# Kernel tuning notes

Hardware: AMD Instinct MI355X
Metric: run time of the kernel (lower is better)

Reference implementation:

```python
import jax, jax.numpy as jnp
import numpy as np

LAT = 4; K = 4; NP = 3 * K - 1; HID = 16; NT = 10; BOUND = 5.0
_in_deg = np.arange(1, LAT + 1)
_hd = (np.arange(HID) % (LAT - 1)) + 1
M1 = jnp.asarray((_hd[:, None] >= _in_deg[None, :]).astype(np.float32))  # [HID, LAT]
M2 = jnp.asarray((_hd[:, None] >= _hd[None, :]).astype(np.float32))      # [HID, HID]
M3 = jnp.asarray((np.repeat(_in_deg, NP)[:, None] > _hd[None, :]).astype(np.float32))  # [LAT*NP, HID]


def _subm(x, m, w, b):
    # submanifold conv: inactive inputs are zero, output restricted to active sites
    y = jax.lax.conv_general_dilated(x, w, (1, 1), 'SAME', dimension_numbers=('NHWC', 'HWIO', 'NHWC')) + b
    return jnp.where(m[..., None], y, 0.0)


def _maxpool(x, m, kh, kw):
    neg = jnp.asarray(-1e30, x.dtype)
    xm = jnp.where(m[..., None], x, neg)
    y = jax.lax.reduce_window(xm, neg, jax.lax.max, (1, kh, kw, 1), (1, kh, kw, 1), 'VALID')
    mo = jax.lax.reduce_window(m.astype(x.dtype), 0.0, jax.lax.max, (1, kh, kw), (1, kh, kw), 'VALID') > 0
    return jnp.where(mo[..., None], y, 0.0), mo


def _invconv(x, w, b, mo):
    # sparse inverse conv with kernel == stride of paired pool: non-overlapping transposed conv
    kh, kw, ci, co = w.shape
    B, h, wd, _ = x.shape
    y = jnp.einsum('bhwc,ijcd->bhiwjd', x, w).reshape(B, h * kh, wd * kw, co) + b
    return jnp.where(mo[..., None], y, 0.0)


def _rqs(x, uw, uh, ud):
    # monotonic rational-quadratic spline, identity outside [-BOUND, BOUND]
    shp = x.shape
    widths = jax.nn.softmax(uw, -1) * (2 * BOUND)
    heights = jax.nn.softmax(uh, -1) * (2 * BOUND)
    edge = jnp.full(shp + (1,), -BOUND, x.dtype)
    xk = jnp.concatenate([edge, jnp.cumsum(widths, -1) - BOUND], -1)
    yk = jnp.concatenate([edge, jnp.cumsum(heights, -1) - BOUND], -1)
    one = jnp.ones(shp + (1,), x.dtype)
    dk = jnp.concatenate([one, jax.nn.softplus(ud), one], -1)
    inside = (x >= -BOUND) & (x <= BOUND)
    xc = jnp.clip(x, -BOUND, BOUND)
    idx = jnp.clip(jnp.sum((xc[..., None] >= xk[..., :-1]).astype(jnp.int32), -1) - 1, 0, K - 1)[..., None]
    g = lambda a, i: jnp.take_along_axis(a, i, -1)[..., 0]
    x0, x1 = g(xk, idx), g(xk, idx + 1)
    y0, y1 = g(yk, idx), g(yk, idx + 1)
    d0, d1 = g(dk, idx), g(dk, idx + 1)
    dx = x1 - x0
    dy = y1 - y0
    s = dy / dx
    t = (xc - x0) / dx
    den = s + (d1 + d0 - 2 * s) * t * (1 - t)
    y = y0 + dy * (s * t * t + d0 * t * (1 - t)) / den
    ld = jnp.log(s * s * (d1 * t * t + 2 * s * t * (1 - t) + d0 * (1 - t) ** 2)) - 2 * jnp.log(den)
    return jnp.where(inside, y, x), jnp.where(inside, ld, 0.0)


def _nsf(z, fW1, fb1, fW2, fb2, fW3, fb3):
    ld_tot = jnp.zeros(z.shape[:-1], z.dtype)
    for t in range(NT):
        h = jax.nn.relu(z @ (fW1[t] * M1).T + fb1[t])
        h = jax.nn.relu(h @ (fW2[t] * M2).T + fb2[t])
        p = (h @ (fW3[t] * M3).T + fb3[t]).reshape(z.shape[:-1] + (LAT, NP))
        z, ld = _rqs(z, p[..., :K], p[..., K:2 * K], p[..., 2 * K:])
        ld_tot = ld_tot + ld.sum(-1)
        if t < NT - 1:
            z = z[..., ::-1]
    return z, ld_tot


def _forward(x, eps, w1, b1, w2, b2, w3, b3, wmu, bmu, wlv, blv, wlin, blin, u1, bu1, w4, b4, u2, bu2, w5, b5, u3, bu3, w6, b6, fW1, fb1, fW2, fb2, fW3, fb3):
    xn = jnp.transpose(x, (0, 2, 3, 1))  # NCHW -> NHWC
    m0 = jnp.any(xn != 0, axis=-1)       # active sites (spconv from_dense)
    lrelu = lambda v: jax.nn.leaky_relu(v, 0.01)
    y = lrelu(_subm(xn, m0, w1, b1))
    y, m1 = _maxpool(y, m0, 2, 2)
    y = lrelu(_subm(y, m1, w2, b2))
    y, m2 = _maxpool(y, m1, 5, 2)
    y = lrelu(_subm(y, m2, w3, b3))
    y, m3 = _maxpool(y, m2, 5, 2)        # [B, 4, 16, 32]
    mu = jnp.where(m3[..., None], y @ wmu.T + bmu, 0.0)
    logvar = jnp.where(m3[..., None], y @ wlv.T + blv, 0.0)
    std = jnp.exp(0.5 * logvar)
    z0 = mu + eps * std
    z, log_det = _nsf(z0, fW1, fb1, fW2, fb2, fW3, fb3)
    LOG2PI = 1.8378770664093453
    log_q0 = jnp.sum(-0.5 * ((z0 - mu) / std) ** 2 - jnp.log(std) - 0.5 * LOG2PI, -1)
    log_p = jnp.sum(-0.5 * z * z - 0.5 * LOG2PI, -1)
    kld_pc = log_q0 - log_det - log_p
    kld = jnp.sum(jnp.where(m3, kld_pc, 0.0), axis=(1, 2))  # index_add over batch indices
    zf = jnp.where(m3[..., None], z, 0.0)
    dec = jnp.where(m3[..., None], zf @ wlin.T + blin, 0.0)
    y = _invconv(dec, u1, bu1, m2)
    y = _subm(y, m2, w4, b4)
    y = _invconv(y, u2, bu2, m1)
    y = _subm(y, m1, w5, b5)
    y = _invconv(y, u3, bu3, m0)
    y = _subm(y, m0, w6, b6)
    out = jnp.transpose(y, (0, 3, 1, 2))  # back to NCHW like .dense()
    return out, mu, logvar, kld, zf


def setup_inputs():
    key = jax.random.key(0)
    ks = iter(jax.random.split(key, 80))
    B, C, H, W = 128, 6, 200, 128
    d = {}
    x = jax.random.normal(next(ks), (B, C, H, W), jnp.float32)
    keep = jax.random.uniform(next(ks), (B, 1, H, W)) < 0.15
    d['x'] = jnp.where(keep, x, 0.0)
    d['eps'] = jax.random.normal(next(ks), (B, 4, 16, LAT), jnp.float32)
    def p(name, shape, s=0.1):
        d[name] = jax.random.normal(next(ks), shape, jnp.float32) * s
    p('w1', (3, 3, 6, 8)); p('b1', (8,))
    p('w2', (3, 3, 8, 16)); p('b2', (16,))
    p('w3', (3, 3, 16, 32)); p('b3', (32,))
    p('wmu', (LAT, 32)); p('bmu', (LAT,))
    p('wlv', (LAT, 32)); p('blv', (LAT,))
    p('wlin', (32, LAT)); p('blin', (32,))
    p('u1', (5, 2, 32, 32)); p('bu1', (32,))
    p('w4', (3, 3, 32, 16)); p('b4', (16,))
    p('u2', (5, 2, 16, 16)); p('bu2', (16,))
    p('w5', (3, 3, 16, 8)); p('b5', (8,))
    p('u3', (2, 2, 8, 8)); p('bu3', (8,))
    p('w6', (3, 3, 8, 6)); p('b6', (6,))
    p('fW1', (NT, HID, LAT)); p('fb1', (NT, HID))
    p('fW2', (NT, HID, HID)); p('fb2', (NT, HID))
    p('fW3', (NT, LAT * NP, HID)); p('fb3', (NT, LAT * NP))
    return d


def reference(x, eps, w1, b1, w2, b2, w3, b3, wmu, bmu, wlv, blv, wlin, blin, u1, bu1, w4, b4, u2, bu2, w5, b5, u3, bu3, w6, b6, fW1, fb1, fW2, fb2, fW3, fb3):
    return _forward(x, eps, w1, b1, w2, b2, w3, b3, wmu, bmu, wlv, blv, wlin, blin, u1, bu1, w4, b4, u2, bu2, w5, b5, u3, bu3, w6, b6, fW1, fb1, fW2, fb2, fW3, fb3)
```

## Files before the change

kernel.cpp:

```cpp
#include <hip/hip_runtime.h>
#include <math.h>

constexpr int NB=128;
constexpr int NH0=200, NW0=128, NC0=6;
constexpr int NH1=100, NW1=64,  NC1=8;
constexpr int NH2=20,  NW2=32,  NC2=16;
constexpr int NH3=4,   NW3=16,  NC3=32;
constexpr int LAT=4, NPp=11, HID=16, NT=10;
constexpr float BOUNDf=5.0f;
constexpr float LOG2PI=1.8378770664093453f;

__device__ __forceinline__ float fexpf(float v){ return __expf(v); }
__device__ __forceinline__ float flogf(float v){ return __logf(v); }
__device__ __forceinline__ float softplusf(float v){ return v>20.f ? v : __logf(1.f+__expf(v)); }
__device__ __forceinline__ float lrelu(float v){ return v>0.f ? v : 0.01f*v; }

__global__ __launch_bounds__(256) void k_conv1pool(
    const float* __restrict__ x, const float* __restrict__ w1, const float* __restrict__ b1,
    float* __restrict__ y1p, unsigned char* __restrict__ m0, unsigned char* __restrict__ m1){
  __shared__ float xs[6][34][34];
  __shared__ float ws1[54][8];
  __shared__ unsigned char ms[34][34];
  int blk = blockIdx.x;
  int b  = blk / 28;
  int t  = blk % 28;
  int th = t / 4, tw = t % 4;
  int hp0 = th*16, wp0 = tw*16;
  int h0 = hp0*2 - 1, w0 = wp0*2 - 1;
  int tid = threadIdx.x;
  for (int i=tid;i<432;i+=256) ws1[i>>3][i&7] = w1[i];
  for (int i=tid;i<6*34*34;i+=256){
    int ci=i/1156; int rem=i-ci*1156; int r=rem/34, c=rem-r*34;
    int h=h0+r, w=w0+c;
    float v=0.f;
    if (h>=0 && h<NH0 && w>=0 && w<NW0) v = x[((size_t)(b*NC0+ci)*NH0+h)*NW0+w];
    xs[ci][r][c]=v;
  }
  __syncthreads();
  for (int i=tid;i<1156;i+=256){
    int r=i/34, c=i-r*34;
    bool any=false;
    #pragma unroll
    for (int ci=0;ci<6;ci++) any |= (xs[ci][r][c]!=0.f);
    ms[r][c] = any?1:0;
  }
  __syncthreads();
  for (int i=tid;i<1024;i+=256){
    int r=(i>>5)+1, c=(i&31)+1;
    int h=h0+r, w=w0+c;
    if (h<NH0) m0[(b*NH0+h)*NW0+w] = ms[r][c];
  }
  int lhp = tid>>4, lwp = tid&15;
  int hp = hp0+lhp, wp = wp0+lwp;
  if (hp < NH1){
    float best[8];
    #pragma unroll
    for (int co=0;co<8;co++) best[co]=-1e30f;
    bool many=false;
    #pragma unroll 1
    for (int i=0;i<2;i++)
    #pragma unroll 1
    for (int j=0;j<2;j++){
      int r = lhp*2+i+1, c = lwp*2+j+1;
      if (!ms[r][c]) continue;
      many=true;
      float a[8];
      #pragma unroll
      for (int co=0;co<8;co++) a[co]=b1[co];
      #pragma unroll 1
      for (int kh=0;kh<3;kh++)
      #pragma unroll 1
      for (int kw=0;kw<3;kw++){
        #pragma unroll
        for (int ci=0;ci<6;ci++){
          float v = xs[ci][r-1+kh][c-1+kw];
          const float* wv = ws1[(kh*3+kw)*6+ci];
          #pragma unroll
          for (int co=0;co<8;co++) a[co]=fmaf(v,wv[co],a[co]);
        }
      }
      #pragma unroll
      for (int co=0;co<8;co++) best[co]=fmaxf(best[co], lrelu(a[co]));
    }
    float* yp = y1p + (((size_t)b*NH1+hp)*NW1+wp)*8;
    #pragma unroll
    for (int co=0;co<8;co++) yp[co] = many?best[co]:0.f;
    m1[(b*NH1+hp)*NW1+wp] = many?1:0;
  }
}

__global__ __launch_bounds__(256) void k_conv2pool(
    const float* __restrict__ yin, const unsigned char* __restrict__ m1,
    const float* __restrict__ w2, const float* __restrict__ b2,
    float* __restrict__ yout, unsigned char* __restrict__ m2){
  __shared__ float ys[8][27][35];
  __shared__ unsigned char msl[27][35];
  __shared__ float w2s[72][16];
  __shared__ float b2s[16];
  int blk = blockIdx.x;
  int b  = blk >> 3;
  int t  = blk & 7;
  int th = t >> 1, tw = t & 1;
  int r0 = th*25 - 1, c0 = tw*32 - 1;
  int tid = threadIdx.x;
  for (int i=tid;i<1152;i+=256) w2s[i>>4][i&15] = w2[i];
  if (tid<16) b2s[tid]=b2[tid];
  for (int p=tid;p<27*34;p+=256){
    int r=p/34, c=p-(p/34)*34;
    int h1=r0+r, w1c=c0+c;
    bool ok = (h1>=0 && h1<NH1 && w1c>=0 && w1c<NW1);
    msl[r][c] = ok ? m1[(b*NH1+h1)*NW1+w1c] : 0;
    float4 v0=make_float4(0,0,0,0), v1=v0;
    if (ok){
      const float4* pp = (const float4*)(yin + (((size_t)b*NH1+h1)*NW1+w1c)*8);
      v0=pp[0]; v1=pp[1];
    }
    ys[0][r][c]=v0.x; ys[1][r][c]=v0.y; ys[2][r][c]=v0.z; ys[3][r][c]=v0.w;
    ys[4][r][c]=v1.x; ys[5][r][c]=v1.y; ys[6][r][c]=v1.z; ys[7][r][c]=v1.w;
  }
  __syncthreads();
  if (tid < 160){
    int oid = tid >> 1, coq = tid & 1;
    int co0 = coq*8;
    int lh = oid >> 4, lw = oid & 15;
    int h2 = th*5+lh, w2c = tw*16+lw;
    float best[8];
    #pragma unroll
    for (int co=0;co<8;co++) best[co]=-1e30f;
    bool many=false;
    #pragma unroll 1
    for (int i=0;i<5;i++)
    #pragma unroll 1
    for (int j=0;j<2;j++){
      int r = lh*5+i+1, c = lw*2+j+1;
      if (!msl[r][c]) continue;
      many=true;
      float a[8];
      #pragma unroll
      for (int co=0;co<8;co++) a[co]=b2s[co0+co];
      #pragma unroll 1
      for (int kh=0;kh<3;kh++)
      #pragma unroll 1
      for (int kw=0;kw<3;kw++){
        #pragma unroll
        for (int ci=0;ci<8;ci++){
          float v = ys[ci][r-1+kh][c-1+kw];
          const float* wr = w2s[(kh*3+kw)*8+ci];
          #pragma unroll
          for (int co=0;co<8;co++) a[co]=fmaf(v,wr[co0+co],a[co]);
        }
      }
      #pragma unroll
      for (int co=0;co<8;co++) best[co]=fmaxf(best[co], lrelu(a[co]));
    }
    float4 o0,o1;
    if (many){
      o0=make_float4(best[0],best[1],best[2],best[3]);
      o1=make_float4(best[4],best[5],best[6],best[7]);
    } else { o0=make_float4(0,0,0,0); o1=o0; }
    float4* op = (float4*)(yout + (((size_t)b*NH2+h2)*NW2+w2c)*16 + co0);
    op[0]=o0; op[1]=o1;
    if (coq==0) m2[(b*NH2+h2)*NW2+w2c] = many?1:0;
  }
}

__global__ __launch_bounds__(256) void k_conv3pool(
    const float* __restrict__ yin, const unsigned char* __restrict__ m2,
    const float* __restrict__ w3, const float* __restrict__ b3,
    float* __restrict__ yout, unsigned char* __restrict__ m3){
  __shared__ float ys[16][20][33];
  __shared__ unsigned char msl[20][32];
  __shared__ float w3s[144][32];
  __shared__ float b3s[32];
  int b = blockIdx.x;
  int tid = threadIdx.x;
  for (int i=tid;i<4608;i+=256) w3s[i>>5][i&31] = w3[i];
  if (tid<32) b3s[tid]=b3[tid];
  for (int p=tid;p<640;p+=256){
    int r=p>>5, c=p&31;
    msl[r][c] = m2[(b*NH2+r)*NW2+c];
    const float4* pp = (const float4*)(yin + (((size_t)b*NH2+r)*NW2+c)*16);
    float4 q0=pp[0],q1=pp[1],q2=pp[2],q3=pp[3];
    ys[0][r][c]=q0.x; ys[1][r][c]=q0.y; ys[2][r][c]=q0.z; ys[3][r][c]=q0.w;
    ys[4][r][c]=q1.x; ys[5][r][c]=q1.y; ys[6][r][c]=q1.z; ys[7][r][c]=q1.w;
    ys[8][r][c]=q2.x; ys[9][r][c]=q2.y; ys[10][r][c]=q2.z; ys[11][r][c]=q2.w;
    ys[12][r][c]=q3.x; ys[13][r][c]=q3.y; ys[14][r][c]=q3.z; ys[15][r][c]=q3.w;
  }
  __syncthreads();
  int p = tid>>2, coq = tid&3;
  int co0 = coq*8;
  int hp = p>>4, wp = p&15;
  float best[8];
  #pragma unroll
  for (int co=0;co<8;co++) best[co]=-1e30f;
  bool many=false;
  #pragma unroll 1
  for (int i=0;i<5;i++)
  #pragma unroll 1
  for (int j=0;j<2;j++){
    int h2 = hp*5+i, w2c = wp*2+j;
    if (!msl[h2][w2c]) continue;
    many=true;
    float a[8];
    #pragma unroll
    for (int co=0;co<8;co++) a[co]=b3s[co0+co];
    #pragma unroll 1
    for (int kh=0;kh<3;kh++){
      int hh=h2+kh-1;
      if (hh<0||hh>=NH2) continue;
      #pragma unroll 1
      for (int kw=0;kw<3;kw++){
        int ww=w2c+kw-1;
        if (ww<0||ww>=NW2) continue;
        #pragma unroll
        for (int ci=0;ci<16;ci++){
          float v = ys[ci][hh][ww];
          const float* wr = w3s[(kh*3+kw)*16+ci];
          #pragma unroll
          for (int co=0;co<8;co++) a[co]=fmaf(v,wr[co0+co],a[co]);
        }
      }
    }
    #pragma unroll
    for (int co=0;co<8;co++) best[co]=fmaxf(best[co], lrelu(a[co]));
  }
  float4 o0,o1;
  if (many){
    o0=make_float4(best[0],best[1],best[2],best[3]);
    o1=make_float4(best[4],best[5],best[6],best[7]);
  } else { o0=make_float4(0,0,0,0); o1=o0; }
  float4* op = (float4*)(yout + ((size_t)(b*64+p))*32 + co0);
  op[0]=o0; op[1]=o1;
  if (coq==0) m3[b*64+p] = many?1:0;
}

__global__ __launch_bounds__(64) void k_latent(
    const float* __restrict__ y3p, const unsigned char* __restrict__ m3,
    const float* __restrict__ eps,
    const float* __restrict__ wmu, const float* __restrict__ bmu,
    const float* __restrict__ wlv, const float* __restrict__ blv,
    const float* __restrict__ wlin, const float* __restrict__ blin,
    const float* __restrict__ fW1, const float* __restrict__ fb1,
    const float* __restrict__ fW2, const float* __restrict__ fb2,
    const float* __restrict__ fW3, const float* __restrict__ fb3,
    float* __restrict__ out_mu, float* __restrict__ out_lv,
    float* __restrict__ out_kld, float* __restrict__ out_zf,
    float* __restrict__ dec)
{
  __shared__ __align__(16) float sW1[NT*HID*LAT];
  __shared__ float sb1[NT*HID];
  __shared__ __align__(16) float sW2[NT*HID*HID];
  __shared__ float sb2[NT*HID];
  __shared__ __align__(16) float sW3[NT*LAT*NPp*HID];
  __shared__ float sb3[NT*LAT*NPp];
  __shared__ float red[64];
  int tid = threadIdx.x;
  for (int i=tid;i<NT*HID*LAT;i+=64){ int j=i&3; int r=(i>>2)%HID; sW1[i]=fW1[i]*(((r%3+1)>=(j+1))?1.f:0.f); }
  for (int i=tid;i<NT*HID;i+=64){ sb1[i]=fb1[i]; sb2[i]=fb2[i]; }
  for (int i=tid;i<NT*HID*HID;i+=64){ int j=i&15; int r=(i>>4)%HID; sW2[i]=fW2[i]*(((r%3+1)>=(j%3+1))?1.f:0.f); }
  for (int i=tid;i<NT*LAT*NPp*HID;i+=64){ int j=i&15; int r=(i>>4)%(LAT*NPp); sW3[i]=fW3[i]*(((r/NPp+1)>(j%3+1))?1.f:0.f); }
  for (int i=tid;i<NT*LAT*NPp;i+=64) sb3[i]=fb3[i];
  __syncthreads();

  int b = blockIdx.x;
  int gpos = b*64 + tid;
  bool msk = m3[gpos]!=0;
  float kld_pc=0.f;
  if (msk){
    float yv[NC3];
    const float* yp = y3p + (size_t)gpos*NC3;
    #pragma unroll
    for (int c=0;c<NC3;c++) yv[c]=yp[c];
    float muv[LAT], lvv[LAT], stdv[LAT], evv[LAT], z0[LAT], z[LAT];
    #pragma unroll
    for (int l=0;l<LAT;l++){
      float a=bmu[l], g=blv[l];
      #pragma unroll
      for (int c=0;c<NC3;c++){ a=fmaf(yv[c],wmu[l*NC3+c],a); g=fmaf(yv[c],wlv[l*NC3+c],g); }
      muv[l]=a; lvv[l]=g;
      stdv[l]=fexpf(0.5f*g);
      evv[l]=eps[(size_t)gpos*LAT+l];
      z0[l]=fmaf(evv[l], stdv[l], a);
      z[l]=z0[l];
    }
    float ld_tot=0.f;
    for (int t=0;t<NT;t++){
      float h1[HID], h2[HID];
      const float* W1t = sW1 + t*HID*LAT;
      const float* b1t = sb1 + t*HID;
      float4 zv = make_float4(z[0],z[1],z[2],z[3]);
      #pragma unroll
      for (int i2=0;i2<HID;i2++){
        float4 wr = *(const float4*)(W1t + i2*4);
        float a = b1t[i2];
        a = fmaf(zv.x,wr.x, fmaf(zv.y,wr.y, fmaf(zv.z,wr.z, fmaf(zv.w,wr.w, a))));
        h1[i2]=fmaxf(a,0.f);
      }
      const float* W2t = sW2 + t*HID*HID;
      const float* b2t = sb2 + t*HID;
      #pragma unroll
      for (int i2=0;i2<HID;i2++){
        float a=b2t[i2];
        const float4* wr = (const float4*)(W2t + i2*HID);
        #pragma unroll
        for (int q=0;q<4;q++){
          float4 w4 = wr[q];
          a = fmaf(h1[q*4+0],w4.x, fmaf(h1[q*4+1],w4.y, fmaf(h1[q*4+2],w4.z, fmaf(h1[q*4+3],w4.w, a))));
        }
        h2[i2]=fmaxf(a,0.f);
      }
      const float* W3t = sW3 + t*LAT*NPp*HID;
      const float* b3t = sb3 + t*LAT*NPp;
      float zn[LAT];
      #pragma unroll
      for (int l=0;l<LAT;l++){
        float p[NPp];
        #pragma unroll
        for (int r=0;r<NPp;r++){
          int rr=l*NPp+r;
          float a=b3t[rr];
          const float4* wr = (const float4*)(W3t + rr*HID);
          #pragma unroll
          for (int q=0;q<4;q++){
            float4 w4 = wr[q];
            a = fmaf(h2[q*4+0],w4.x, fmaf(h2[q*4+1],w4.y, fmaf(h2[q*4+2],w4.z, fmaf(h2[q*4+3],w4.w, a))));
          }
          p[r]=a;
        }
        float mw=fmaxf(fmaxf(p[0],p[1]),fmaxf(p[2],p[3]));
        float e0=fexpf(p[0]-mw), e1=fexpf(p[1]-mw), e2=fexpf(p[2]-mw), e3=fexpf(p[3]-mw);
        float wsc=10.f/(e0+e1+e2+e3);
        float xk1=fmaf(e0,wsc,-BOUNDf), xk2=fmaf(e1,wsc,xk1), xk3=fmaf(e2,wsc,xk2), xk4=fmaf(e3,wsc,xk3);
        float mh=fmaxf(fmaxf(p[4],p[5]),fmaxf(p[6],p[7]));
        float f0=fexpf(p[4]-mh), f1=fexpf(p[5]-mh), f2=fexpf(p[6]-mh), f3=fexpf(p[7]-mh);
        float hsc=10.f/(f0+f1+f2+f3);
        float yk1=fmaf(f0,hsc,-BOUNDf), yk2=fmaf(f1,hsc,yk1), yk3=fmaf(f2,hsc,yk2), yk4=fmaf(f3,hsc,yk3);
        float dk1=softplusf(p[8]), dk2=softplusf(p[9]), dk3=softplusf(p[10]);
        float xv=z[l];
        bool inside = (xv>=-BOUNDf)&&(xv<=BOUNDf);
        float xc=fminf(fmaxf(xv,-BOUNDf),BOUNDf);
        float x0=-BOUNDf, x1=xk1, y0=-BOUNDf, y1=yk1, d0=1.f, d1=dk1;
        if (xc>=xk1){x0=xk1;x1=xk2;y0=yk1;y1=yk2;d0=dk1;d1=dk2;}
        if (xc>=xk2){x0=xk2;x1=xk3;y0=yk2;y1=yk3;d0=dk2;d1=dk3;}
        if (xc>=xk3){x0=xk3;x1=xk4;y0=yk3;y1=yk4;d0=dk3;d1=1.f;}
        float dxv=x1-x0, dyv=y1-y0;
        float sl=dyv/dxv, ttv=(xc-x0)/dxv, omt=1.f-ttv;
        float den=sl + (d1+d0-2.f*sl)*ttv*omt;
        float yo=y0 + dyv*(sl*ttv*ttv + d0*ttv*omt)/den;
        float ldv=flogf(sl*sl*(d1*ttv*ttv + 2.f*sl*ttv*omt + d0*omt*omt)) - 2.f*flogf(den);
        zn[l] = inside ? yo : xv;
        ld_tot += inside ? ldv : 0.f;
      }
      if (t<NT-1){ z[0]=zn[3]; z[1]=zn[2]; z[2]=zn[1]; z[3]=zn[0]; }
      else       { z[0]=zn[0]; z[1]=zn[1]; z[2]=zn[2]; z[3]=zn[3]; }
    }
    float lq=0.f, lp=0.f;
    #pragma unroll
    for (int l=0;l<LAT;l++){
      lq += -0.5f*evv[l]*evv[l] - 0.5f*lvv[l] - 0.5f*LOG2PI;
      lp += -0.5f*z[l]*z[l] - 0.5f*LOG2PI;
    }
    kld_pc = lq - ld_tot - lp;
    #pragma unroll
    for (int l=0;l<LAT;l++){
      out_mu[(size_t)gpos*LAT+l]=muv[l];
      out_lv[(size_t)gpos*LAT+l]=lvv[l];
      out_zf[(size_t)gpos*LAT+l]=z[l];
    }
    #pragma unroll
    for (int k2=0;k2<NC3;k2++){
      float a=blin[k2];
      #pragma unroll
      for (int l=0;l<LAT;l++) a=fmaf(z[l],wlin[k2*LAT+l],a);
      dec[(size_t)gpos*NC3+k2]=a;
    }
  } else {
    #pragma unroll
    for (int l=0;l<LAT;l++){
      out_mu[(size_t)gpos*LAT+l]=0.f;
      out_lv[(size_t)gpos*LAT+l]=0.f;
      out_zf[(size_t)gpos*LAT+l]=0.f;
    }
    for (int k2=0;k2<NC3;k2++) dec[(size_t)gpos*NC3+k2]=0.f;
  }
  red[tid]=kld_pc;
  __syncthreads();
  for (int s=32;s>0;s>>=1){ if (tid<s) red[tid]+=red[tid+s]; __syncthreads(); }
  if (tid==0) out_kld[b]=red[0];
}

__global__ __launch_bounds__(256) void k_ic4(
    const float* __restrict__ dec, const unsigned char* __restrict__ m2,
    const float* __restrict__ u1, const float* __restrict__ bu1,
    const float* __restrict__ w4, const float* __restrict__ b4,
    float* __restrict__ t2){
  __shared__ __align__(16) float vs[12][18][32];
  __shared__ __align__(16) float w4s[288][16];
  __shared__ unsigned char msl[12][18];
  int blk = blockIdx.x;
  int b  = blk >> 2;
  int t  = blk & 3;
  int th = t >> 1, tw = t & 1;
  int h0 = th*10, w0 = tw*16;
  int tid = threadIdx.x;
  for (int i=tid;i<288*16;i+=256) w4s[i>>4][i&15] = w4[i];
  if (tid < 216){
    int lr = tid/18, lc = tid%18;
    int h2 = h0-1+lr, w2 = w0-1+lc;
    bool mk = (h2>=0 && h2<NH2 && w2>=0 && w2<NW2) && m2[(b*NH2+h2)*NW2+w2];
    msl[lr][lc] = mk?1:0;
    float acc[32];
    if (mk){
      const float* dp = dec + (((size_t)b*NH3 + h2/5)*NW3 + w2/2)*NC3;
      const float* up = u1 + ((h2%5)*2 + (w2&1))*1024;
      #pragma unroll
      for (int co=0;co<32;co++) acc[co]=bu1[co];
      #pragma unroll 1
      for (int ci=0;ci<32;ci++){
        float dv = dp[ci];
        const float* ur = up + ci*32;
        #pragma unroll
        for (int co=0;co<32;co++) acc[co]=fmaf(dv,ur[co],acc[co]);
      }
    } else {
      #pragma unroll
      for (int co=0;co<32;co++) acc[co]=0.f;
    }
    #pragma unroll
    for (int co=0;co<32;co++) vs[lr][lc][co]=acc[co];
  }
  __syncthreads();
  if (tid < 160){
    int lh = tid/16, lw = tid%16;
    int h2 = h0+lh, w2 = w0+lw;
    float a[16];
    if (msl[lh+1][lw+1]){
      #pragma unroll
      for (int co=0;co<16;co++) a[co]=b4[co];
      #pragma unroll 1
      for (int kh=0;kh<3;kh++)
      #pragma unroll 1
      for (int kw=0;kw<3;kw++){
        const float* vp = vs[lh+kh][lw+kw];
        #pragma unroll
        for (int ci=0;ci<32;ci++){
          float v = vp[ci];
          const float* wr = w4s[(kh*3+kw)*32+ci];
          #pragma unroll
          for (int co=0;co<16;co++) a[co]=fmaf(v,wr[co],a[co]);
        }
      }
    } else {
      #pragma unroll
      for (int co=0;co<16;co++) a[co]=0.f;
    }
    float* op = t2 + (((size_t)b*NH2+h2)*NW2+w2)*NC2;
    #pragma unroll
    for (int co=0;co<16;co++) op[co]=a[co];
  }
}

__global__ __launch_bounds__(256) void k_ic5(
    const float* __restrict__ t2, const unsigned char* __restrict__ m1,
    const float* __restrict__ u2, const float* __restrict__ bu2,
    const float* __restrict__ w5, const float* __restrict__ b5,
    float* __restrict__ t4){
  __shared__ __align__(16) float vs[12][18][16];
  __shared__ __align__(16) float w5s[144][8];
  __shared__ unsigned char msl[12][18];
  int blk = blockIdx.x;
  int b  = blk / 40;
  int t  = blk % 40;
  int th = t >> 2, tw = t & 3;
  int h0 = th*10, w0 = tw*16;
  int tid = threadIdx.x;
  for (int i=tid;i<144*8;i+=256) w5s[i>>3][i&7] = w5[i];
  if (tid < 216){
    int lr = tid/18, lc = tid%18;
    int h1 = h0-1+lr, w1c = w0-1+lc;
    bool mk = (h1>=0 && h1<NH1 && w1c>=0 && w1c<NW1) && m1[(b*NH1+h1)*NW1+w1c];
    msl[lr][lc] = mk?1:0;
    float acc[16];
    if (mk){
      const float* dp = t2 + (((size_t)b*NH2 + h1/5)*NW2 + w1c/2)*NC2;
      const float* up = u2 + ((h1%5)*2 + (w1c&1))*256;
      #pragma unroll
      for (int co=0;co<16;co++) acc[co]=bu2[co];
      #pragma unroll 1
      for (int ci=0;ci<16;ci++){
        float dv = dp[ci];
        const float* ur = up + ci*16;
        #pragma unroll
        for (int co=0;co<16;co++) acc[co]=fmaf(dv,ur[co],acc[co]);
      }
    } else {
      #pragma unroll
      for (int co=0;co<16;co++) acc[co]=0.f;
    }
    #pragma unroll
    for (int co=0;co<16;co++) vs[lr][lc][co]=acc[co];
  }
  __syncthreads();
  if (tid < 160){
    int lh = tid/16, lw = tid%16;
    int h1 = h0+lh, w1c = w0+lw;
    float a[8];
    if (msl[lh+1][lw+1]){
      #pragma unroll
      for (int co=0;co<8;co++) a[co]=b5[co];
      #pragma unroll 1
      for (int kh=0;kh<3;kh++)
      #pragma unroll 1
      for (int kw=0;kw<3;kw++){
        const float* vp = vs[lh+kh][lw+kw];
        #pragma unroll
        for (int ci=0;ci<16;ci++){
          float v = vp[ci];
          const float* wr = w5s[(kh*3+kw)*16+ci];
          #pragma unroll
          for (int co=0;co<8;co++) a[co]=fmaf(v,wr[co],a[co]);
        }
      }
    } else {
      #pragma unroll
      for (int co=0;co<8;co++) a[co]=0.f;
    }
    float* op = t4 + (((size_t)b*NH1+h1)*NW1+w1c)*NC1;
    #pragma unroll
    for (int co=0;co<8;co++) op[co]=a[co];
  }
}

__global__ __launch_bounds__(256) void k_inv3conv6(
    const float* __restrict__ t4, const unsigned char* __restrict__ m0,
    const float* __restrict__ u3, const float* __restrict__ bu3,
    const float* __restrict__ w6, const float* __restrict__ b6,
    float* __restrict__ out){
  __shared__ float ts[8][10][36];
  __shared__ unsigned char msl[18][66];
  __shared__ float u3s[4][8][8];
  __shared__ float w6s[9][8][6];
  __shared__ float bu3s[8];
  __shared__ float b6s[6];
  int blk = blockIdx.x;
  int b  = blk / 26;
  int t  = blk % 26;
  int th = t >> 1, tw = t & 1;
  int h0 = th*16, w0 = tw*64;
  int base_r = 8*th - 1, base_c = 32*tw - 1;
  int tid = threadIdx.x;
  for (int i=tid;i<256;i+=256){ int pos=i>>6; int rem=i&63; u3s[pos][rem>>3][rem&7]=u3[i]; }
  for (int i=tid;i<432;i+=256){ int tap=i/48; int rem=i%48; w6s[tap][rem/6][rem%6]=w6[i]; }
  if (tid<8) bu3s[tid]=bu3[tid];
  if (tid<6) b6s[tid]=b6[tid];
  for (int p=tid;p<340;p+=256){
    int r=p/34, c=p-(p/34)*34;
    int h1=base_r+r, w1c=base_c+c;
    float4 v0=make_float4(0,0,0,0), v1=v0;
    if (h1>=0 && h1<NH1 && w1c>=0 && w1c<NW1){
      const float4* pp = (const float4*)(t4 + (((size_t)b*NH1+h1)*NW1+w1c)*8);
      v0=pp[0]; v1=pp[1];
    }
    ts[0][r][c]=v0.x; ts[1][r][c]=v0.y; ts[2][r][c]=v0.z; ts[3][r][c]=v0.w;
    ts[4][r][c]=v1.x; ts[5][r][c]=v1.y; ts[6][r][c]=v1.z; ts[7][r][c]=v1.w;
  }
  for (int p=tid;p<18*66;p+=256){
    int r=p/66, c=p-(p/66)*66;
    int h=h0-1+r, w=w0-1+c;
    msl[r][c] = (h>=0 && h<NH0 && w>=0 && w<NW0) ? m0[(b*NH0+h)*NW0+w] : 0;
  }
  __syncthreads();
  #pragma unroll 1
  for (int k=0;k<4;k++){
    int p = tid + k*256;
    int lh = p>>6, lw = p&63;
    int h = h0+lh, w = w0+lw;
    if (h >= NH0) continue;
    float acc[6];
    if (msl[lh+1][lw+1]){
      #pragma unroll
      for (int co=0;co<6;co++) acc[co]=b6s[co];
      #pragma unroll 1
      for (int kh=0;kh<3;kh++)
      #pragma unroll 1
      for (int kw=0;kw<3;kw++){
        if (!msl[lh+kh][lw+kw]) continue;
        int hh = h+kh-1, ww = w+kw-1;
        int tr = (hh>>1) - base_r, tc = (ww>>1) - base_c;
        int pos = (hh&1)*2 + (ww&1);
        float v8[8];
        #pragma unroll
        for (int c8=0;c8<8;c8++) v8[c8]=bu3s[c8];
        #pragma unroll
        for (int ci=0;ci<8;ci++){
          float v = ts[ci][tr][tc];
          #pragma unroll
          for (int c8=0;c8<8;c8++) v8[c8]=fmaf(v, u3s[pos][ci][c8], v8[c8]);
        }
        const float (*wt)[6] = w6s[kh*3+kw];
        #pragma unroll
        for (int ci=0;ci<8;ci++)
          #pragma unroll
          for (int co=0;co<6;co++) acc[co]=fmaf(v8[ci], wt[ci][co], acc[co]);
      }
    } else {
      #pragma unroll
      for (int co=0;co<6;co++) acc[co]=0.f;
    }
    size_t base = (size_t)b*6*NH0*NW0 + (size_t)h*NW0 + w;
    #pragma unroll
    for (int co=0;co<6;co++) out[base + (size_t)co*NH0*NW0] = acc[co];
  }
}

extern "C" void kernel_launch(void* const* d_in, const int* in_sizes, int n_in,
                              void* d_out, int out_size, void* d_ws, size_t ws_size,
                              hipStream_t stream){
  (void)in_sizes; (void)n_in; (void)out_size; (void)ws_size;
  const float* x    = (const float*)d_in[0];
  const float* eps  = (const float*)d_in[1];
  const float* w1   = (const float*)d_in[2];
  const float* b1   = (const float*)d_in[3];
  const float* w2   = (const float*)d_in[4];
  const float* b2   = (const float*)d_in[5];
  const float* w3   = (const float*)d_in[6];
  const float* b3   = (const float*)d_in[7];
  const float* wmu  = (const float*)d_in[8];
  const float* bmu  = (const float*)d_in[9];
  const float* wlv  = (const float*)d_in[10];
  const float* blv  = (const float*)d_in[11];
  const float* wlin = (const float*)d_in[12];
  const float* blin = (const float*)d_in[13];
  const float* u1   = (const float*)d_in[14];
  const float* bu1  = (const float*)d_in[15];
  const float* w4   = (const float*)d_in[16];
  const float* b4   = (const float*)d_in[17];
  const float* u2   = (const float*)d_in[18];
  const float* bu2  = (const float*)d_in[19];
  const float* w5   = (const float*)d_in[20];
  const float* b5   = (const float*)d_in[21];
  const float* u3   = (const float*)d_in[22];
  const float* bu3  = (const float*)d_in[23];
  const float* w6   = (const float*)d_in[24];
  const float* b6   = (const float*)d_in[25];
  const float* fW1  = (const float*)d_in[26];
  const float* fb1  = (const float*)d_in[27];
  const float* fW2  = (const float*)d_in[28];
  const float* fb2  = (const float*)d_in[29];
  const float* fW3  = (const float*)d_in[30];
  const float* fb3  = (const float*)d_in[31];

  char* ws = (char*)d_ws;
  unsigned char* m0 = (unsigned char*)(ws);
  unsigned char* m1 = (unsigned char*)(ws + 3276800);
  unsigned char* m2 = (unsigned char*)(ws + 4096000);
  unsigned char* m3 = (unsigned char*)(ws + 4177920);
  float* y1p = (float*)(ws + 4194304);
  float* y2p = (float*)(ws + 30408704);
  float* y3p = (float*)(ws + 35651584);
  float* dec = (float*)(ws + 36700160);
  float* t2  = y2p;
  float* t4  = y1p;

  float* out   = (float*)d_out;
  float* o_mu  = out + 19660800;
  float* o_lv  = out + 19693568;
  float* o_kld = out + 19726336;
  float* o_zf  = out + 19726464;

  k_conv1pool<<< 3584,256,0,stream>>>(x, w1, b1, y1p, m0, m1);
  k_conv2pool<<< 1024,256,0,stream>>>(y1p, m1, w2, b2, y2p, m2);
  k_conv3pool<<<  128,256,0,stream>>>(y2p, m2, w3, b3, y3p, m3);
  k_latent   <<<  128, 64,0,stream>>>(y3p, m3, eps, wmu,bmu,wlv,blv,wlin,blin,
                                      fW1,fb1,fW2,fb2,fW3,fb3, o_mu,o_lv,o_kld,o_zf, dec);
  k_ic4      <<<  512,256,0,stream>>>(dec, m2, u1, bu1, w4, b4, t2);
  k_ic5      <<< 5120,256,0,stream>>>(t2, m1, u2, bu2, w5, b5, t4);
  k_inv3conv6<<< 3328,256,0,stream>>>(t4, m0, u3, bu3, w6, b6, out);
}
```

Before: 521.6 us.

## Split latent flow across four lanes per site with shuffle exchange and atomic KLD

The latent/flow kernel now assigns four threads to each spatial site, one per latent dimension, instead of one thread per site. The grid grows from 128 to 512 blocks. Hidden activations and spline outputs are exchanged between the four lanes with xor shuffles. The KLD reduction becomes a wavefront shuffle reduction plus an atomicAdd into an output that conv3pool zero-initialises. This is meant to cut the long serial per-thread chain and the poor occupancy of 128 blocks of 64 threads. The cost is redundant h1 computation in every lane, extra shuffles, and each block still loading the full weight tables into shared memory.

```diff
diff --git a/kernel.cpp b/kernel.cpp
--- a/kernel.cpp
+++ b/kernel.cpp
@@ -167,13 +167,15 @@
 __global__ __launch_bounds__(256) void k_conv3pool(
     const float* __restrict__ yin, const unsigned char* __restrict__ m2,
     const float* __restrict__ w3, const float* __restrict__ b3,
-    float* __restrict__ yout, unsigned char* __restrict__ m3){
+    float* __restrict__ yout, unsigned char* __restrict__ m3,
+    float* __restrict__ out_kld){
   __shared__ float ys[16][20][33];
   __shared__ unsigned char msl[20][32];
   __shared__ float w3s[144][32];
   __shared__ float b3s[32];
   int b = blockIdx.x;
   int tid = threadIdx.x;
+  if (tid==0) out_kld[b]=0.f;
   for (int i=tid;i<4608;i+=256) w3s[i>>5][i&31] = w3[i];
   if (tid<32) b3s[tid]=b3[tid];
   for (int p=tid;p<640;p+=256){
@@ -253,140 +255,156 @@
   __shared__ float sb2[NT*HID];
   __shared__ __align__(16) float sW3[NT*LAT*NPp*HID];
   __shared__ float sb3[NT*LAT*NPp];
-  __shared__ float red[64];
+  __shared__ __align__(16) float swmu[LAT*NC3];
+  __shared__ __align__(16) float swlv[LAT*NC3];
+  __shared__ __align__(16) float slin[NC3*LAT];
+  __shared__ float sbmu[LAT], sblv[LAT], sblin[NC3];
   int tid = threadIdx.x;
   for (int i=tid;i<NT*HID*LAT;i+=64){ int j=i&3; int r=(i>>2)%HID; sW1[i]=fW1[i]*(((r%3+1)>=(j+1))?1.f:0.f); }
   for (int i=tid;i<NT*HID;i+=64){ sb1[i]=fb1[i]; sb2[i]=fb2[i]; }
   for (int i=tid;i<NT*HID*HID;i+=64){ int j=i&15; int r=(i>>4)%HID; sW2[i]=fW2[i]*(((r%3+1)>=(j%3+1))?1.f:0.f); }
   for (int i=tid;i<NT*LAT*NPp*HID;i+=64){ int j=i&15; int r=(i>>4)%(LAT*NPp); sW3[i]=fW3[i]*(((r/NPp+1)>(j%3+1))?1.f:0.f); }
   for (int i=tid;i<NT*LAT*NPp;i+=64) sb3[i]=fb3[i];
-  __syncthreads();
-
-  int b = blockIdx.x;
-  int gpos = b*64 + tid;
+  for (int i=tid;i<LAT*NC3;i+=64){ swmu[i]=wmu[i]; swlv[i]=wlv[i]; slin[i]=wlin[i]; }
+  if (tid<LAT){ sbmu[tid]=bmu[tid]; sblv[tid]=blv[tid]; }
+  for (int i=tid;i<NC3;i+=64) sblin[i]=blin[i];
+  __syncthreads();
+
+  int blk = blockIdx.x;
+  int b   = blk >> 2;
+  int gpos = b*64 + (blk&3)*16 + (tid>>2);
+  int g = tid & 3;
   bool msk = m3[gpos]!=0;
-  float kld_pc=0.f;
+  float kld_part = 0.f;
   if (msk){
-    float yv[NC3];
-    const float* yp = y3p + (size_t)gpos*NC3;
-    #pragma unroll
-    for (int c=0;c<NC3;c++) yv[c]=yp[c];
-    float muv[LAT], lvv[LAT], stdv[LAT], evv[LAT], z0[LAT], z[LAT];
-    #pragma unroll
-    for (int l=0;l<LAT;l++){
-      float a=bmu[l], g=blv[l];
-      #pragma unroll
-      for (int c=0;c<NC3;c++){ a=fmaf(yv[c],wmu[l*NC3+c],a); g=fmaf(yv[c],wlv[l*NC3+c],g); }
-      muv[l]=a; lvv[l]=g;
-      stdv[l]=fexpf(0.5f*g);
-      evv[l]=eps[(size_t)gpos*LAT+l];
-      z0[l]=fmaf(evv[l], stdv[l], a);
-      z[l]=z0[l];
-    }
-    float ld_tot=0.f;
+    const float4* yp = (const float4*)(y3p + (size_t)gpos*NC3);
+    const float4* wm = (const float4*)(swmu + g*NC3);
+    const float4* wl = (const float4*)(swlv + g*NC3);
+    float mu_g = sbmu[g], lv_g = sblv[g];
+    #pragma unroll
+    for (int q=0;q<8;q++){
+      float4 yq = yp[q], a = wm[q], c = wl[q];
+      mu_g = fmaf(yq.x,a.x, fmaf(yq.y,a.y, fmaf(yq.z,a.z, fmaf(yq.w,a.w, mu_g))));
+      lv_g = fmaf(yq.x,c.x, fmaf(yq.y,c.y, fmaf(yq.z,c.z, fmaf(yq.w,c.w, lv_g))));
+    }
+    float std_g = fexpf(0.5f*lv_g);
+    float ev_g  = eps[(size_t)gpos*LAT+g];
+    float z0_g  = fmaf(ev_g, std_g, mu_g);
+    float zg = z0_g;
+    float z[4];
+    z[g]=zg; z[g^1]=__shfl_xor(zg,1); z[g^2]=__shfl_xor(zg,2); z[g^3]=__shfl_xor(zg,3);
+    float ld_g = 0.f;
     for (int t=0;t<NT;t++){
-      float h1[HID], h2[HID];
-      const float* W1t = sW1 + t*HID*LAT;
-      const float* b1t = sb1 + t*HID;
-      float4 zv = make_float4(z[0],z[1],z[2],z[3]);
-      #pragma unroll
-      for (int i2=0;i2<HID;i2++){
-        float4 wr = *(const float4*)(W1t + i2*4);
+      float h1[16];
+      const float4* W1t = (const float4*)(sW1 + t*HID*LAT);
+      const float*  b1t = sb1 + t*HID;
+      #pragma unroll
+      for (int i2=0;i2<16;i2++){
+        float4 w = W1t[i2];
         float a = b1t[i2];
-        a = fmaf(zv.x,wr.x, fmaf(zv.y,wr.y, fmaf(zv.z,wr.z, fmaf(zv.w,wr.w, a))));
+        a = fmaf(z[0],w.x, fmaf(z[1],w.y, fmaf(z[2],w.z, fmaf(z[3],w.w, a))));
         h1[i2]=fmaxf(a,0.f);
       }
+      float h2o[4];
       const float* W2t = sW2 + t*HID*HID;
       const float* b2t = sb2 + t*HID;
       #pragma unroll
-      for (int i2=0;i2<HID;i2++){
-        float a=b2t[i2];
-        const float4* wr = (const float4*)(W2t + i2*HID);
+      for (int k=0;k<4;k++){
+        int row = g*4+k;
+        const float4* wr = (const float4*)(W2t + row*HID);
+        float a = b2t[row];
         #pragma unroll
         for (int q=0;q<4;q++){
-          float4 w4 = wr[q];
-          a = fmaf(h1[q*4+0],w4.x, fmaf(h1[q*4+1],w4.y, fmaf(h1[q*4+2],w4.z, fmaf(h1[q*4+3],w4.w, a))));
-        }
-        h2[i2]=fmaxf(a,0.f);
-      }
+          float4 w = wr[q];
+          a = fmaf(h1[q*4+0],w.x, fmaf(h1[q*4+1],w.y, fmaf(h1[q*4+2],w.z, fmaf(h1[q*4+3],w.w, a))));
+        }
+        h2o[k]=fmaxf(a,0.f);
+      }
+      float h2[16];
+      #pragma unroll
+      for (int k=0;k<4;k++) h2[g*4+k]=h2o[k];
+      #pragma unroll
+      for (int mski=1;mski<4;mski++){
+        int og = g^mski;
+        #pragma unroll
+        for (int k=0;k<4;k++) h2[og*4+k]=__shfl_xor(h2o[k],mski);
+      }
+      float p[NPp];
       const float* W3t = sW3 + t*LAT*NPp*HID;
       const float* b3t = sb3 + t*LAT*NPp;
-      float zn[LAT];
-      #pragma unroll
-      for (int l=0;l<LAT;l++){
-        float p[NPp];
-        #pragma unroll
-        for (int r=0;r<NPp;r++){
-          int rr=l*NPp+r;
-          float a=b3t[rr];
-          const float4* wr = (const float4*)(W3t + rr*HID);
-          #pragma unroll
-          for (int q=0;q<4;q++){
-            float4 w4 = wr[q];
-            a = fmaf(h2[q*4+0],w4.x, fmaf(h2[q*4+1],w4.y, fmaf(h2[q*4+2],w4.z, fmaf(h2[q*4+3],w4.w, a))));
-          }
-          p[r]=a;
-        }
-        float mw=fmaxf(fmaxf(p[0],p[1]),fmaxf(p[2],p[3]));
-        float e0=fexpf(p[0]-mw), e1=fexpf(p[1]-mw), e2=fexpf(p[2]-mw), e3=fexpf(p[3]-mw);
-        float wsc=10.f/(e0+e1+e2+e3);
-        float xk1=fmaf(e0,wsc,-BOUNDf), xk2=fmaf(e1,wsc,xk1), xk3=fmaf(e2,wsc,xk2), xk4=fmaf(e3,wsc,xk3);
-        float mh=fmaxf(fmaxf(p[4],p[5]),fmaxf(p[6],p[7]));
-        float f0=fexpf(p[4]-mh), f1=fexpf(p[5]-mh), f2=fexpf(p[6]-mh), f3=fexpf(p[7]-mh);
-        float hsc=10.f/(f0+f1+f2+f3);
-        float yk1=fmaf(f0,hsc,-BOUNDf), yk2=fmaf(f1,hsc,yk1), yk3=fmaf(f2,hsc,yk2), yk4=fmaf(f3,hsc,yk3);
-        float dk1=softplusf(p[8]), dk2=softplusf(p[9]), dk3=softplusf(p[10]);
-        float xv=z[l];
-        bool inside = (xv>=-BOUNDf)&&(xv<=BOUNDf);
-        float xc=fminf(fmaxf(xv,-BOUNDf),BOUNDf);
-        float x0=-BOUNDf, x1=xk1, y0=-BOUNDf, y1=yk1, d0=1.f, d1=dk1;
-        if (xc>=xk1){x0=xk1;x1=xk2;y0=yk1;y1=yk2;d0=dk1;d1=dk2;}
-        if (xc>=xk2){x0=xk2;x1=xk3;y0=yk2;y1=yk3;d0=dk2;d1=dk3;}
-        if (xc>=xk3){x0=xk3;x1=xk4;y0=yk3;y1=yk4;d0=dk3;d1=1.f;}
-        float dxv=x1-x0, dyv=y1-y0;
-        float sl=dyv/dxv, ttv=(xc-x0)/dxv, omt=1.f-ttv;
-        float den=sl + (d1+d0-2.f*sl)*ttv*omt;
-        float yo=y0 + dyv*(sl*ttv*ttv + d0*ttv*omt)/den;
-        float ldv=flogf(sl*sl*(d1*ttv*ttv + 2.f*sl*ttv*omt + d0*omt*omt)) - 2.f*flogf(den);
-        zn[l] = inside ? yo : xv;
-        ld_tot += inside ? ldv : 0.f;
-      }
-      if (t<NT-1){ z[0]=zn[3]; z[1]=zn[2]; z[2]=zn[1]; z[3]=zn[0]; }
-      else       { z[0]=zn[0]; z[1]=zn[1]; z[2]=zn[2]; z[3]=zn[3]; }
-    }
-    float lq=0.f, lp=0.f;
-    #pragma unroll
-    for (int l=0;l<LAT;l++){
-      lq += -0.5f*evv[l]*evv[l] - 0.5f*lvv[l] - 0.5f*LOG2PI;
-      lp += -0.5f*z[l]*z[l] - 0.5f*LOG2PI;
-    }
-    kld_pc = lq - ld_tot - lp;
-    #pragma unroll
-    for (int l=0;l<LAT;l++){
-      out_mu[(size_t)gpos*LAT+l]=muv[l];
-      out_lv[(size_t)gpos*LAT+l]=lvv[l];
-      out_zf[(size_t)gpos*LAT+l]=z[l];
-    }
-    #pragma unroll
-    for (int k2=0;k2<NC3;k2++){
-      float a=blin[k2];
-      #pragma unroll
-      for (int l=0;l<LAT;l++) a=fmaf(z[l],wlin[k2*LAT+l],a);
-      dec[(size_t)gpos*NC3+k2]=a;
-    }
+      #pragma unroll
+      for (int r=0;r<NPp;r++){
+        int row = g*NPp+r;
+        const float4* wr = (const float4*)(W3t + row*HID);
+        float a = b3t[row];
+        #pragma unroll
+        for (int q=0;q<4;q++){
+          float4 w = wr[q];
+          a = fmaf(h2[q*4+0],w.x, fmaf(h2[q*4+1],w.y, fmaf(h2[q*4+2],w.z, fmaf(h2[q*4+3],w.w, a))));
+        }
+        p[r]=a;
+      }
+      float mw=fmaxf(fmaxf(p[0],p[1]),fmaxf(p[2],p[3]));
+      float e0=fexpf(p[0]-mw), e1=fexpf(p[1]-mw), e2=fexpf(p[2]-mw), e3=fexpf(p[3]-mw);
+      float wsc=10.f/(e0+e1+e2+e3);
+      float xk1=fmaf(e0,wsc,-BOUNDf), xk2=fmaf(e1,wsc,xk1), xk3=fmaf(e2,wsc,xk2), xk4=fmaf(e3,wsc,xk3);
+      float mh=fmaxf(fmaxf(p[4],p[5]),fmaxf(p[6],p[7]));
+      float f0=fexpf(p[4]-mh), f1=fexpf(p[5]-mh), f2=fexpf(p[6]-mh), f3=fexpf(p[7]-mh);
+      float hsc=10.f/(f0+f1+f2+f3);
+      float yk1=fmaf(f0,hsc,-BOUNDf), yk2=fmaf(f1,hsc,yk1), yk3=fmaf(f2,hsc,yk2), yk4=fmaf(f3,hsc,yk3);
+      float dk1=softplusf(p[8]), dk2=softplusf(p[9]), dk3=softplusf(p[10]);
+      float xv=z[g];
+      bool inside = (xv>=-BOUNDf)&&(xv<=BOUNDf);
+      float xc=fminf(fmaxf(xv,-BOUNDf),BOUNDf);
+      float x0=-BOUNDf, x1=xk1, y0=-BOUNDf, y1=yk1, d0=1.f, d1=dk1;
+      if (xc>=xk1){x0=xk1;x1=xk2;y0=yk1;y1=yk2;d0=dk1;d1=dk2;}
+      if (xc>=xk2){x0=xk2;x1=xk3;y0=yk2;y1=yk3;d0=dk2;d1=dk3;}
+      if (xc>=xk3){x0=xk3;x1=xk4;y0=yk3;y1=yk4;d0=dk3;d1=1.f;}
+      float dxv=x1-x0, dyv=y1-y0;
+      float sl=dyv/dxv, ttv=(xc-x0)/dxv, omt=1.f-ttv;
+      float den=sl + (d1+d0-2.f*sl)*ttv*omt;
+      float yo=y0 + dyv*(sl*ttv*ttv + d0*ttv*omt)/den;
+      float ldv=flogf(sl*sl*(d1*ttv*ttv + 2.f*sl*ttv*omt + d0*omt*omt)) - 2.f*flogf(den);
+      float zn_g = inside ? yo : xv;
+      ld_g += inside ? ldv : 0.f;
+      float znf[4];
+      znf[g]=zn_g; znf[g^1]=__shfl_xor(zn_g,1); znf[g^2]=__shfl_xor(zn_g,2); znf[g^3]=__shfl_xor(zn_g,3);
+      if (t<NT-1){ z[0]=znf[3]; z[1]=znf[2]; z[2]=znf[1]; z[3]=znf[0]; }
+      else       { z[0]=znf[0]; z[1]=znf[1]; z[2]=znf[2]; z[3]=znf[3]; }
+    }
+    float lq_g = -0.5f*ev_g*ev_g - 0.5f*lv_g - 0.5f*LOG2PI;
+    float lp_g = -0.5f*z[g]*z[g] - 0.5f*LOG2PI;
+    kld_part = lq_g - ld_g - lp_g;
+    out_mu[(size_t)gpos*LAT+g]=mu_g;
+    out_lv[(size_t)gpos*LAT+g]=lv_g;
+    out_zf[(size_t)gpos*LAT+g]=z[g];
+    float4 d0v, d1v;
+    {
+      float dv[8];
+      #pragma unroll
+      for (int k=0;k<8;k++){
+        int c = g*8+k;
+        const float4 w = ((const float4*)slin)[c];
+        dv[k] = fmaf(z[0],w.x, fmaf(z[1],w.y, fmaf(z[2],w.z, fmaf(z[3],w.w, sblin[c]))));
+      }
+      d0v=make_float4(dv[0],dv[1],dv[2],dv[3]);
+      d1v=make_float4(dv[4],dv[5],dv[6],dv[7]);
+    }
+    float4* dp = (float4*)(dec + (size_t)gpos*NC3 + g*8);
+    dp[0]=d0v; dp[1]=d1v;
   } else {
-    #pragma unroll
-    for (int l=0;l<LAT;l++){
-      out_mu[(size_t)gpos*LAT+l]=0.f;
-      out_lv[(size_t)gpos*LAT+l]=0.f;
-      out_zf[(size_t)gpos*LAT+l]=0.f;
-    }
-    for (int k2=0;k2<NC3;k2++) dec[(size_t)gpos*NC3+k2]=0.f;
-  }
-  red[tid]=kld_pc;
-  __syncthreads();
-  for (int s=32;s>0;s>>=1){ if (tid<s) red[tid]+=red[tid+s]; __syncthreads(); }
-  if (tid==0) out_kld[b]=red[0];
+    out_mu[(size_t)gpos*LAT+g]=0.f;
+    out_lv[(size_t)gpos*LAT+g]=0.f;
+    out_zf[(size_t)gpos*LAT+g]=0.f;
+    float4 zv = make_float4(0,0,0,0);
+    float4* dp = (float4*)(dec + (size_t)gpos*NC3 + g*8);
+    dp[0]=zv; dp[1]=zv;
+  }
+  float s = kld_part;
+  s += __shfl_xor(s,1);  s += __shfl_xor(s,2);
+  s += __shfl_xor(s,4);  s += __shfl_xor(s,8);
+  s += __shfl_xor(s,16); s += __shfl_xor(s,32);
+  if (tid==0) atomicAdd(&out_kld[b], s);
 }
 
 __global__ __launch_bounds__(256) void k_ic4(
@@ -670,8 +688,8 @@
 
   k_conv1pool<<< 3584,256,0,stream>>>(x, w1, b1, y1p, m0, m1);
   k_conv2pool<<< 1024,256,0,stream>>>(y1p, m1, w2, b2, y2p, m2);
-  k_conv3pool<<<  128,256,0,stream>>>(y2p, m2, w3, b3, y3p, m3);
-  k_latent   <<<  128, 64,0,stream>>>(y3p, m3, eps, wmu,bmu,wlv,blv,wlin,blin,
+  k_conv3pool<<<  128,256,0,stream>>>(y2p, m2, w3, b3, y3p, m3, o_kld);
+  k_latent   <<<  512, 64,0,stream>>>(y3p, m3, eps, wmu,bmu,wlv,blv,wlin,blin,
                                       fW1,fb1,fW2,fb2,fW3,fb3, o_mu,o_lv,o_kld,o_zf, dec);
   k_ic4      <<<  512,256,0,stream>>>(dec, m2, u1, bu1, w4, b4, t2);
   k_ic5      <<< 5120,256,0,stream>>>(t2, m1, u2, bu2, w5, b5, t4);
```

After: 482.0 us. 7.6% less time.
